# Kernel tuning notes

Measured on AMD Instinct MI355X. Metric: run time of the kernel, lower is better.

Reference implementation:

```python
import jax, jax.numpy as jnp
import numpy as np

B, N, H = 4, 200, 300


def setup_inputs() -> dict:
    key = jax.random.key(0)
    ks = jax.random.split(key, 6)
    s = 1.0 / np.sqrt(H)
    return {
        "x": jax.random.normal(ks[0], (B, N, H), dtype=jnp.float32),
        "e": jax.random.normal(ks[1], (B, N, N, H), dtype=jnp.float32),
        "U_w": jax.random.uniform(ks[2], (H, H), jnp.float32, -s, s),
        "U_b": jax.random.uniform(ks[3], (H,), jnp.float32, -s, s),
        "V_w": jax.random.uniform(ks[4], (H, H), jnp.float32, -s, s),
        "V_b": jax.random.uniform(ks[5], (H,), jnp.float32, -s, s),
    }


def reference(x, e, U_w, U_b, V_w, V_b):
    # Ue = e @ U_w.T + U_b  -> (B, N, N, H)
    Ue = jnp.einsum("bijh,gh->bijg", e, U_w) + U_b
    # Vx = x @ V_w.T + V_b  -> (B, N, H)
    Vx = jnp.einsum("bnh,gh->bng", x, V_w) + V_b
    # e_new[b,i,j] = Ue[b,i,j] + Vx[b,i] + Vx[b,j]
    e_new = Ue + Vx[:, :, None, :] + Vx[:, None, :, :]
    return e_new
```

## Files before the change

kernel.cpp:

```cpp
#include <hip/hip_runtime.h>
#include <hip/hip_bf16.h>

#define BB 4
#define NN 200
#define HH 300
#define NCH 10
#define GF 20
#define BM 64

typedef __attribute__((ext_vector_type(8))) short short8;
typedef __attribute__((ext_vector_type(4))) float float4v;

static __device__ __forceinline__ ushort f2bf(float x) {
    union { float f; uint u; } v; v.f = x;
    uint r = v.u + 0x7FFFu + ((v.u >> 16) & 1u);
    return (ushort)(r >> 16);
}

static __device__ __forceinline__ short8 pack8_cvt(float4v a, float4v b) {
    uint u0, u1, u2, u3;
    asm("v_cvt_pk_bf16_f32 %0, %1, %2" : "=v"(u0) : "v"(a[0]), "v"(a[1]));
    asm("v_cvt_pk_bf16_f32 %0, %1, %2" : "=v"(u1) : "v"(a[2]), "v"(a[3]));
    asm("v_cvt_pk_bf16_f32 %0, %1, %2" : "=v"(u2) : "v"(b[0]), "v"(b[1]));
    asm("v_cvt_pk_bf16_f32 %0, %1, %2" : "=v"(u3) : "v"(b[2]), "v"(b[3]));
    union { uint u[4]; short8 s; } r;
    r.u[0] = u0; r.u[1] = u1; r.u[2] = u2; r.u[3] = u3;
    return r.s;
}

static __device__ __forceinline__ void gload_lds16(const void* g, void* l) {
    __builtin_amdgcn_global_load_lds(
        (const __attribute__((address_space(1))) unsigned int*)g,
        (__attribute__((address_space(3))) unsigned int*)l, 16, 0, 0);
}

__global__ void pack_u(const float* __restrict__ Uw, ushort* __restrict__ Bp) {
    int idx = blockIdx.x * 256 + threadIdx.x;
    if (idx >= NCH * GF * 64) return;
    int lane = idx & 63;
    int kg = idx >> 6;
    int gf = kg % GF, ks = kg / GF;
    int g = gf * 16 + (lane & 15);
    int h0 = ks * 32 + (lane >> 4) * 8;
    ushort v[8];
#pragma unroll
    for (int j = 0; j < 8; ++j) {
        int h = h0 + j;
        v[j] = (g < HH && h < HH) ? f2bf(Uw[g * HH + h]) : (ushort)0;
    }
    *reinterpret_cast<short8*>(Bp + (size_t)idx * 8) = *reinterpret_cast<const short8*>(v);
}

__global__ void vx_kernel(const float* __restrict__ x, const float* __restrict__ Vw,
                          const float* __restrict__ Vb, const float* __restrict__ Ub,
                          float* __restrict__ Vx) {
    __shared__ float xs[HH];
    int row = blockIdx.x;
    const float* xr = x + (size_t)row * HH;
    for (int h = threadIdx.x; h < HH; h += 256) xs[h] = xr[h];
    __syncthreads();
    for (int g = threadIdx.x; g < HH; g += 256) {
        const float4* wr = reinterpret_cast<const float4*>(Vw + (size_t)g * HH);
        const float4* xv = reinterpret_cast<const float4*>(xs);
        float s0 = 0.f, s1 = 0.f, s2 = 0.f, s3 = 0.f;
#pragma unroll 5
        for (int k = 0; k < HH / 4; ++k) {
            float4 w = wr[k];
            float4 xx = xv[k];
            s0 += w.x * xx.x; s1 += w.y * xx.y; s2 += w.z * xx.z; s3 += w.w * xx.w;
        }
        Vx[(size_t)row * HH + g] = Vb[g] + 0.5f * Ub[g] + s0 + s1 + s2 + s3;
    }
}

__launch_bounds__(256, 3)
__global__ void gemm_kernel(const float* __restrict__ e, const ushort* __restrict__ Bp,
                            const float* __restrict__ Vx, float* __restrict__ out) {
    __shared__ __align__(16) ushort Alds[2][BM * 32];
    __shared__ __align__(16) ushort Blds[2][GF * 512];
    const int tid = threadIdx.x;
    const int w = tid >> 6, l = tid & 63;
    const int r = l & 15, q = l >> 4;
    const int m0 = blockIdx.x * BM;
    const int arow = tid >> 2;
    const int acg = tid & 3;
    const float* rowp = e + (size_t)(m0 + arow) * HH;
    const int awidx = ((arow >> 4) * 64 + (arow & 15) + acg * 16) * 8;

    float4v s0a, s0b, s1a, s1b, s2a, s2b;

    float4v acc[GF];
#pragma unroll
    for (int f = 0; f < GF; ++f) acc[f] = (float4v){0.f, 0.f, 0.f, 0.f};

#define LOAD_A(K_, S_) do {                                                     \
        int c0_ = (K_) * 32 + acg * 8;                                          \
        const float* p0_ = (c0_ + 4 <= HH) ? rowp + c0_ : e;                    \
        const float* p1_ = (c0_ + 8 <= HH) ? rowp + c0_ + 4 : e;                \
        S_##a = *reinterpret_cast<const float4v*>(p0_);                         \
        S_##b = *reinterpret_cast<const float4v*>(p1_);                         \
    } while (0)

#define WRITE_A(K_, S_, P_) do {                                                \
        short8 w_ = pack8_cvt(S_##a, S_##b);                                    \
        if ((K_) == 9) {                                                        \
            _Pragma("unroll")                                                   \
            for (int j_ = 0; j_ < 8; ++j_)                                      \
                if (288 + acg * 8 + j_ >= HH) w_[j_] = 0;                       \
        }                                                                       \
        *reinterpret_cast<short8*>(&Alds[P_][awidx]) = w_;                      \
    } while (0)

#define ISSUE_B(K_, P_) do {                                                    \
        const char* bs_ = (const char*)Bp + (size_t)(K_) * (GF * 1024);         \
        char* bd_ = (char*)&Blds[P_][0];                                        \
        _Pragma("unroll")                                                       \
        for (int rd_ = 0; rd_ < 5; ++rd_)                                       \
            gload_lds16(bs_ + rd_ * 4096 + tid * 16, bd_ + rd_ * 4096 + tid * 16); \
    } while (0)

#define COMPUTE(P_) do {                                                        \
        short8 fa_ = *reinterpret_cast<const short8*>(&Alds[P_][(w * 64 + l) * 8]); \
        const ushort* bb_ = &Blds[P_][l * 8];                                   \
        _Pragma("unroll")                                                       \
        for (int f_ = 0; f_ < GF; ++f_) {                                       \
            short8 bf_ = *reinterpret_cast<const short8*>(bb_ + f_ * 512);      \
            acc[f_] = __builtin_amdgcn_mfma_f32_16x16x32_bf16(bf_, fa_, acc[f_], 0, 0, 0); \
        }                                                                       \
    } while (0)

#define WAITV(N_) do {                                                          \
        __builtin_amdgcn_sched_barrier(0);                                      \
        asm volatile("s_waitcnt vmcnt(" #N_ ")" ::: "memory");                  \
        __builtin_amdgcn_sched_barrier(0);                                      \
    } while (0)

#define ENDPHASE() do {                                                         \
        asm volatile("s_waitcnt lgkmcnt(0)" ::: "memory");                      \
        __builtin_amdgcn_s_barrier();                                           \
        __builtin_amdgcn_sched_barrier(0);                                      \
    } while (0)

    LOAD_A(0, s0); ISSUE_B(0, 0); LOAD_A(1, s1); LOAD_A(2, s2);
    WRITE_A(0, s0, 0);
    WAITV(2);
    ENDPHASE();

    WRITE_A(1, s1, 1); ISSUE_B(1, 1); LOAD_A(3, s0); COMPUTE(0); WAITV(2); ENDPHASE();
    WRITE_A(2, s2, 0); ISSUE_B(2, 0); LOAD_A(4, s1); COMPUTE(1); WAITV(2); ENDPHASE();
    WRITE_A(3, s0, 1); ISSUE_B(3, 1); LOAD_A(5, s2); COMPUTE(0); WAITV(2); ENDPHASE();
    WRITE_A(4, s1, 0); ISSUE_B(4, 0); LOAD_A(6, s0); COMPUTE(1); WAITV(2); ENDPHASE();
    WRITE_A(5, s2, 1); ISSUE_B(5, 1); LOAD_A(7, s1); COMPUTE(0); WAITV(2); ENDPHASE();
    WRITE_A(6, s0, 0); ISSUE_B(6, 0); LOAD_A(8, s2); COMPUTE(1); WAITV(2); ENDPHASE();
    WRITE_A(7, s1, 1); ISSUE_B(7, 1); LOAD_A(9, s0); COMPUTE(0); WAITV(2); ENDPHASE();
    WRITE_A(8, s2, 0); ISSUE_B(8, 0);                COMPUTE(1); WAITV(0); ENDPHASE();
    WRITE_A(9, s0, 1); ISSUE_B(9, 1);                COMPUTE(0); WAITV(0); ENDPHASE();
    COMPUTE(1);

    {
        const int mrow = m0 + w * 16 + r;
        int j = mrow % NN;
        int ti = mrow / NN;
        int b = ti / NN;
        const float* vi = Vx + (size_t)ti * HH;
        const float* vj = Vx + (size_t)(b * NN + j) * HH;
        float* orow = out + (size_t)mrow * HH;
#pragma unroll
        for (int f = 0; f < GF - 1; ++f) {
            int g0 = f * 16 + q * 4;
            if (g0 + 4 <= HH) {
                float4v vi4 = *reinterpret_cast<const float4v*>(vi + g0);
                float4v vj4 = *reinterpret_cast<const float4v*>(vj + g0);
                *reinterpret_cast<float4v*>(orow + g0) = acc[f] + vi4 + vj4;
            }
        }
    }
#undef LOAD_A
#undef WRITE_A
#undef ISSUE_B
#undef COMPUTE
#undef WAITV
#undef ENDPHASE
}

extern "C" void kernel_launch(void* const* d_in, const int* in_sizes, int n_in,
                              void* d_out, int out_size, void* d_ws, size_t ws_size,
                              hipStream_t stream) {
    const float* x  = (const float*)d_in[0];
    const float* e  = (const float*)d_in[1];
    const float* Uw = (const float*)d_in[2];
    const float* Ub = (const float*)d_in[3];
    const float* Vw = (const float*)d_in[4];
    const float* Vb = (const float*)d_in[5];
    float* out = (float*)d_out;

    ushort* Bp = (ushort*)d_ws;
    float*  Vx = (float*)((char*)d_ws + 204800);

    pack_u<<<50, 256, 0, stream>>>(Uw, Bp);
    vx_kernel<<<BB * NN, 256, 0, stream>>>(x, Vw, Vb, Ub, Vx);
    gemm_kernel<<<160000 / BM, 256, 0, stream>>>(e, Bp, Vx, out);
}
```

Before: 166.3 us.

## Split GEMM output columns across two blocks to raise occupancy

```diff
diff --git a/kernel.cpp b/kernel.cpp
--- a/kernel.cpp
+++ b/kernel.cpp
@@ -5,7 +5,7 @@
 #define NN 200
 #define HH 300
 #define NCH 10
-#define GF 20
+#define GHF 10
 #define BM 64
 
 typedef __attribute__((ext_vector_type(8))) short short8;
@@ -36,11 +36,13 @@
 
 __global__ void pack_u(const float* __restrict__ Uw, ushort* __restrict__ Bp) {
     int idx = blockIdx.x * 256 + threadIdx.x;
-    if (idx >= NCH * GF * 64) return;
+    if (idx >= 2 * NCH * GHF * 64) return;
     int lane = idx & 63;
-    int kg = idx >> 6;
-    int gf = kg % GF, ks = kg / GF;
-    int g = gf * 16 + (lane & 15);
+    int rem = idx >> 6;
+    int fh = rem % GHF;
+    int ks = (rem / GHF) % NCH;
+    int gh = rem / (GHF * NCH);
+    int g = (gh * GHF + fh) * 16 + (lane & 15);
     int h0 = ks * 32 + (lane >> 4) * 8;
     ushort v[8];
 #pragma unroll
@@ -73,25 +75,27 @@
     }
 }
 
-__launch_bounds__(256, 3)
+__launch_bounds__(256, 5)
 __global__ void gemm_kernel(const float* __restrict__ e, const ushort* __restrict__ Bp,
                             const float* __restrict__ Vx, float* __restrict__ out) {
     __shared__ __align__(16) ushort Alds[2][BM * 32];
-    __shared__ __align__(16) ushort Blds[2][GF * 512];
+    __shared__ __align__(16) ushort Blds[2][GHF * 512];
     const int tid = threadIdx.x;
     const int w = tid >> 6, l = tid & 63;
     const int r = l & 15, q = l >> 4;
-    const int m0 = blockIdx.x * BM;
+    const int gh = blockIdx.x & 1;
+    const int m0 = (blockIdx.x >> 1) * BM;
     const int arow = tid >> 2;
     const int acg = tid & 3;
     const float* rowp = e + (size_t)(m0 + arow) * HH;
     const int awidx = ((arow >> 4) * 64 + (arow & 15) + acg * 16) * 8;
+    const char* bbase = (const char*)Bp + (size_t)gh * (NCH * GHF * 1024);
 
     float4v s0a, s0b, s1a, s1b, s2a, s2b;
 
-    float4v acc[GF];
+    float4v acc[GHF];
 #pragma unroll
-    for (int f = 0; f < GF; ++f) acc[f] = (float4v){0.f, 0.f, 0.f, 0.f};
+    for (int f = 0; f < GHF; ++f) acc[f] = (float4v){0.f, 0.f, 0.f, 0.f};
 
 #define LOAD_A(K_, S_) do {                                                     \
         int c0_ = (K_) * 32 + acg * 8;                                          \
@@ -112,18 +116,19 @@
     } while (0)
 
 #define ISSUE_B(K_, P_) do {                                                    \
-        const char* bs_ = (const char*)Bp + (size_t)(K_) * (GF * 1024);         \
+        const char* bs_ = bbase + (size_t)(K_) * (GHF * 1024);                  \
         char* bd_ = (char*)&Blds[P_][0];                                        \
-        _Pragma("unroll")                                                       \
-        for (int rd_ = 0; rd_ < 5; ++rd_)                                       \
-            gload_lds16(bs_ + rd_ * 4096 + tid * 16, bd_ + rd_ * 4096 + tid * 16); \
+        gload_lds16(bs_ + tid * 16,        bd_ + tid * 16);                     \
+        gload_lds16(bs_ + 4096 + tid * 16, bd_ + 4096 + tid * 16);              \
+        if (tid < 128)                                                          \
+            gload_lds16(bs_ + 8192 + tid * 16, bd_ + 8192 + tid * 16);          \
     } while (0)
 
 #define COMPUTE(P_) do {                                                        \
         short8 fa_ = *reinterpret_cast<const short8*>(&Alds[P_][(w * 64 + l) * 8]); \
         const ushort* bb_ = &Blds[P_][l * 8];                                   \
         _Pragma("unroll")                                                       \
-        for (int f_ = 0; f_ < GF; ++f_) {                                       \
+        for (int f_ = 0; f_ < GHF; ++f_) {                                      \
             short8 bf_ = *reinterpret_cast<const short8*>(bb_ + f_ * 512);      \
             acc[f_] = __builtin_amdgcn_mfma_f32_16x16x32_bf16(bf_, fa_, acc[f_], 0, 0, 0); \
         }                                                                       \
@@ -165,9 +170,10 @@
         const float* vi = Vx + (size_t)ti * HH;
         const float* vj = Vx + (size_t)(b * NN + j) * HH;
         float* orow = out + (size_t)mrow * HH;
+        const int gbase = gh * (GHF * 16);
 #pragma unroll
-        for (int f = 0; f < GF - 1; ++f) {
-            int g0 = f * 16 + q * 4;
+        for (int f = 0; f < GHF; ++f) {
+            int g0 = gbase + f * 16 + q * 4;
             if (g0 + 4 <= HH) {
                 float4v vi4 = *reinterpret_cast<const float4v*>(vi + g0);
                 float4v vj4 = *reinterpret_cast<const float4v*>(vj + g0);
@@ -199,5 +205,5 @@
 
     pack_u<<<50, 256, 0, stream>>>(Uw, Bp);
     vx_kernel<<<BB * NN, 256, 0, stream>>>(x, Vw, Vb, Ub, Vx);
-    gemm_kernel<<<160000 / BM, 256, 0, stream>>>(e, Bp, Vx, out);
-}
+    gemm_kernel<<<5000, 256, 0, stream>>>(e, Bp, Vx, out);
+}
```

Result: slower. 185.0 us (+11.2%).

## Load A fragments directly into registers, dropping LDS staging for A

Applied to the files above, without the earlier changes.

```diff
diff --git a/kernel.cpp b/kernel.cpp
--- a/kernel.cpp
+++ b/kernel.cpp
@@ -76,42 +76,28 @@
 __launch_bounds__(256, 3)
 __global__ void gemm_kernel(const float* __restrict__ e, const ushort* __restrict__ Bp,
                             const float* __restrict__ Vx, float* __restrict__ out) {
-    __shared__ __align__(16) ushort Alds[2][BM * 32];
     __shared__ __align__(16) ushort Blds[2][GF * 512];
     const int tid = threadIdx.x;
     const int w = tid >> 6, l = tid & 63;
     const int r = l & 15, q = l >> 4;
     const int m0 = blockIdx.x * BM;
-    const int arow = tid >> 2;
-    const int acg = tid & 3;
-    const float* rowp = e + (size_t)(m0 + arow) * HH;
-    const int awidx = ((arow >> 4) * 64 + (arow & 15) + acg * 16) * 8;
-
-    float4v s0a, s0b, s1a, s1b, s2a, s2b;
+    const float* rowp = e + (size_t)(m0 + w * 16 + r) * HH;
 
     float4v acc[GF];
 #pragma unroll
     for (int f = 0; f < GF; ++f) acc[f] = (float4v){0.f, 0.f, 0.f, 0.f};
 
+    float4v e0a, e0b, e1a, e1b;
+
 #define LOAD_A(K_, S_) do {                                                     \
-        int c0_ = (K_) * 32 + acg * 8;                                          \
+        int c0_ = (K_) * 32 + q * 8;                                            \
         const float* p0_ = (c0_ + 4 <= HH) ? rowp + c0_ : e;                    \
         const float* p1_ = (c0_ + 8 <= HH) ? rowp + c0_ + 4 : e;                \
         S_##a = *reinterpret_cast<const float4v*>(p0_);                         \
         S_##b = *reinterpret_cast<const float4v*>(p1_);                         \
     } while (0)
 
-#define WRITE_A(K_, S_, P_) do {                                                \
-        short8 w_ = pack8_cvt(S_##a, S_##b);                                    \
-        if ((K_) == 9) {                                                        \
-            _Pragma("unroll")                                                   \
-            for (int j_ = 0; j_ < 8; ++j_)                                      \
-                if (288 + acg * 8 + j_ >= HH) w_[j_] = 0;                       \
-        }                                                                       \
-        *reinterpret_cast<short8*>(&Alds[P_][awidx]) = w_;                      \
-    } while (0)
-
-#define ISSUE_B(K_, P_) do {                                                    \
+#define STAGE_B(K_, P_) do {                                                    \
         const char* bs_ = (const char*)Bp + (size_t)(K_) * (GF * 1024);         \
         char* bd_ = (char*)&Blds[P_][0];                                        \
         _Pragma("unroll")                                                       \
@@ -119,8 +105,14 @@
             gload_lds16(bs_ + rd_ * 4096 + tid * 16, bd_ + rd_ * 4096 + tid * 16); \
     } while (0)
 
-#define COMPUTE(P_) do {                                                        \
-        short8 fa_ = *reinterpret_cast<const short8*>(&Alds[P_][(w * 64 + l) * 8]); \
+#define COMPUTE(K_, P_, S_) do {                                                \
+        short8 fa_ = pack8_cvt(S_##a, S_##b);                                   \
+        if ((K_) == 9) {                                                        \
+            int c0_ = 288 + q * 8;                                              \
+            _Pragma("unroll")                                                   \
+            for (int j_ = 0; j_ < 8; ++j_)                                      \
+                if (c0_ + j_ >= HH) fa_[j_] = 0;                                \
+        }                                                                       \
         const ushort* bb_ = &Blds[P_][l * 8];                                   \
         _Pragma("unroll")                                                       \
         for (int f_ = 0; f_ < GF; ++f_) {                                       \
@@ -129,42 +121,41 @@
         }                                                                       \
     } while (0)
 
-#define WAITV(N_) do {                                                          \
+#define ENDPHASE() do {                                                         \
         __builtin_amdgcn_sched_barrier(0);                                      \
-        asm volatile("s_waitcnt vmcnt(" #N_ ")" ::: "memory");                  \
-        __builtin_amdgcn_sched_barrier(0);                                      \
-    } while (0)
-
-#define ENDPHASE() do {                                                         \
-        asm volatile("s_waitcnt lgkmcnt(0)" ::: "memory");                      \
+        asm volatile("s_waitcnt vmcnt(0)" ::: "memory");                        \
         __builtin_amdgcn_s_barrier();                                           \
         __builtin_amdgcn_sched_barrier(0);                                      \
     } while (0)
 
-    LOAD_A(0, s0); ISSUE_B(0, 0); LOAD_A(1, s1); LOAD_A(2, s2);
-    WRITE_A(0, s0, 0);
-    WAITV(2);
+    STAGE_B(0, 0); LOAD_A(0, e0);
     ENDPHASE();
 
-    WRITE_A(1, s1, 1); ISSUE_B(1, 1); LOAD_A(3, s0); COMPUTE(0); WAITV(2); ENDPHASE();
-    WRITE_A(2, s2, 0); ISSUE_B(2, 0); LOAD_A(4, s1); COMPUTE(1); WAITV(2); ENDPHASE();
-    WRITE_A(3, s0, 1); ISSUE_B(3, 1); LOAD_A(5, s2); COMPUTE(0); WAITV(2); ENDPHASE();
-    WRITE_A(4, s1, 0); ISSUE_B(4, 0); LOAD_A(6, s0); COMPUTE(1); WAITV(2); ENDPHASE();
-    WRITE_A(5, s2, 1); ISSUE_B(5, 1); LOAD_A(7, s1); COMPUTE(0); WAITV(2); ENDPHASE();
-    WRITE_A(6, s0, 0); ISSUE_B(6, 0); LOAD_A(8, s2); COMPUTE(1); WAITV(2); ENDPHASE();
-    WRITE_A(7, s1, 1); ISSUE_B(7, 1); LOAD_A(9, s0); COMPUTE(0); WAITV(2); ENDPHASE();
-    WRITE_A(8, s2, 0); ISSUE_B(8, 0);                COMPUTE(1); WAITV(0); ENDPHASE();
-    WRITE_A(9, s0, 1); ISSUE_B(9, 1);                COMPUTE(0); WAITV(0); ENDPHASE();
-    COMPUTE(1);
+#define PHASE(T_, P_, SC_, SN_) do {                                            \
+        if ((T_) < 9) { STAGE_B((T_) + 1, (P_) ^ 1); LOAD_A((T_) + 1, SN_); }   \
+        COMPUTE(T_, P_, SC_);                                                   \
+        if ((T_) < 9) ENDPHASE();                                               \
+    } while (0)
+
+    PHASE(0, 0, e0, e1);
+    PHASE(1, 1, e1, e0);
+    PHASE(2, 0, e0, e1);
+    PHASE(3, 1, e1, e0);
+    PHASE(4, 0, e0, e1);
+    PHASE(5, 1, e1, e0);
+    PHASE(6, 0, e0, e1);
+    PHASE(7, 1, e1, e0);
+    PHASE(8, 0, e0, e1);
+    PHASE(9, 1, e1, e0);
 
     {
-        const int mrow = m0 + w * 16 + r;
-        int j = mrow % NN;
-        int ti = mrow / NN;
+        const int m = m0 + w * 16 + r;
+        int j = m % NN;
+        int ti = m / NN;
         int b = ti / NN;
         const float* vi = Vx + (size_t)ti * HH;
         const float* vj = Vx + (size_t)(b * NN + j) * HH;
-        float* orow = out + (size_t)mrow * HH;
+        float* orow = out + (size_t)m * HH;
 #pragma unroll
         for (int f = 0; f < GF - 1; ++f) {
             int g0 = f * 16 + q * 4;
@@ -176,11 +167,10 @@
         }
     }
 #undef LOAD_A
-#undef WRITE_A
-#undef ISSUE_B
+#undef STAGE_B
 #undef COMPUTE
-#undef WAITV
 #undef ENDPHASE
+#undef PHASE
 }
 
 extern "C" void kernel_launch(void* const* d_in, const int* in_sizes, int n_in,
```

New measurement: 160.9 us. 3.3% less time.
